# Kernel tuning notes

Measured on AMD Instinct MI355X. Metric: run time of the kernel, lower is better.

The kernel has to match this reference:

```python
import jax, jax.numpy as jnp
import numpy as np

N_EXPERTS = 8
D_HEAD = 64  # scaling dim (per-expert sub-dim)


def setup_inputs() -> dict:
    key = jax.random.key(0)
    k1, k2, k3, k4, k5, k6 = jax.random.split(key, 6)
    B, H, T, D = 2, 8, 2048, 512
    Q = jax.random.normal(k1, (B, H, T, D), dtype=jnp.float32)
    K = jax.random.normal(k2, (B, H, T, D), dtype=jnp.float32)
    V = jax.random.normal(k3, (B, H, T, D), dtype=jnp.float32)
    route_mat = jax.random.uniform(k4, (B, N_EXPERTS), dtype=jnp.float32)
    ids = jax.random.randint(k5, (B, N_EXPERTS), 0, 8, dtype=jnp.int32)
    mask = jax.random.randint(k6, (T, T), 0, 2, dtype=jnp.int32)
    return {"Q": Q, "K": K, "V": V, "route_mat": route_mat, "ids": ids, "mask": mask}


def reference(Q, K, V, route_mat, ids, mask):
    B, H, T, D = Q.shape
    E = N_EXPERTS
    ds = D // E
    # split feature dim into expert sub-slices: [B,H,T,E,ds]
    Qe = Q.reshape(B, H, T, E, ds)
    Ke = K.reshape(B, H, T, E, ds)
    Ve = V.reshape(B, H, T, E, ds)
    gate = route_mat[:, None, None, :, None]  # [B,1,1,E,1]
    # Row-parallel routed QK^T: sum over experts of gated partial products.
    dot = jnp.einsum('bhqed,bhked->bhqk', Qe * gate, Ke) / np.sqrt(D_HEAD).astype(np.float32)
    dot = jnp.where(mask[None, None, :, :].astype(bool), -jnp.inf, dot)
    attn = jax.nn.softmax(dot, axis=-1)  # dropout p=0.0 (eval)
    # Column-parallel routed score@V: per-expert output gated, concatenated along feature dim.
    Xe = jnp.einsum('bhqk,bhked->bhqed', attn, Ve) * gate
    return Xe.reshape(B, H, T, D)
```

## Files before the change

### kernel.cpp

```cpp
#include <hip/hip_runtime.h>
#include <stdint.h>

#define T_SEQ 2048
#define D_DIM 512
#define NEXP 8

typedef short bf16x8 __attribute__((ext_vector_type(8)));
typedef float floatx4 __attribute__((ext_vector_type(4)));

__device__ __forceinline__ unsigned short f2bf(float f) {
  union { float f; unsigned u; } v; v.f = f;
  return (unsigned short)((v.u + 0x7fffu + ((v.u >> 16) & 1u)) >> 16);
}

__global__ __launch_bounds__(256) void prep_k(const float* __restrict__ K,
                                              unsigned short* __restrict__ kws) {
  int idx = blockIdx.x * 256 + threadIdx.x;
  int r = idx >> 6;
  int c = idx & 63;
  const float4* src = (const float4*)(K + ((long)r << 9) + (c << 3));
  float4 a = src[0], b = src[1];
  bf16x8 v;
  v[0]=f2bf(a.x); v[1]=f2bf(a.y); v[2]=f2bf(a.z); v[3]=f2bf(a.w);
  v[4]=f2bf(b.x); v[5]=f2bf(b.y); v[6]=f2bf(b.z); v[7]=f2bf(b.w);
  int pos = (c ^ (r & 7)) << 4;
  *(bf16x8*)((char*)kws + ((long)r << 10) + pos) = v;
}

__global__ __launch_bounds__(256) void prep_vt(const float* __restrict__ V,
                                               unsigned short* __restrict__ vt) {
  __shared__ unsigned short tile[64][72];
  int bid = blockIdx.x;
  int bh = bid >> 8;
  int kt = (bid >> 3) & 31;
  int dt = bid & 7;
  int k0 = kt << 6, d0 = dt << 6;
  int tid = threadIdx.x;
  {
    int kl = tid >> 2, dc = (tid & 3) << 4;
    const float4* src = (const float4*)(V + ((long)(bh * T_SEQ + k0 + kl) << 9) + d0 + dc);
#pragma unroll
    for (int i = 0; i < 4; ++i) {
      float4 a = src[i];
      tile[kl][dc + 4*i + 0] = f2bf(a.x);
      tile[kl][dc + 4*i + 1] = f2bf(a.y);
      tile[kl][dc + 4*i + 2] = f2bf(a.z);
      tile[kl][dc + 4*i + 3] = f2bf(a.w);
    }
  }
  __syncthreads();
  {
    int dl = tid >> 2, kc = (tid & 3) << 4;
    int d = d0 + dl;
    int swz = ((d ^ (d >> 2)) & 3) << 4;
    long rowbase = (long)(bh * 512 + d) << 12;
#pragma unroll
    for (int m = 0; m < 2; ++m) {
      bf16x8 v;
#pragma unroll
      for (int j = 0; j < 8; ++j) v[j] = tile[kc + 8*m + j][dl];
      int ks = k0 + kc + 8*m;
      int pos = ((ks >> 5) << 6) + ((((ks & 31) << 1)) ^ swz);
      *(bf16x8*)((char*)vt + rowbase + pos) = v;
    }
  }
}

__global__ __launch_bounds__(512, 2) void attn_main(
    const float* __restrict__ Q, const float* __restrict__ route,
    const int* __restrict__ mask, const unsigned short* __restrict__ kws,
    const unsigned short* __restrict__ vtw, float* __restrict__ out) {
  __shared__ __align__(16) char lds[65536];
  const int tid = threadIdx.x;
  const int wq = tid >> 6;
  const int lane = tid & 63;
  const int lq = lane & 15;
  const int g = lane >> 4;
  const int bh = blockIdx.x & 15;
  const int qb = blockIdx.x >> 4;
  const int qw = qb * 128 + wq * 16;
  const int b = bh >> 3;

  float g8[NEXP];
#pragma unroll
  for (int e = 0; e < NEXP; ++e) g8[e] = route[b * NEXP + e];

  bf16x8 qa[16];
  {
    const float* qrow = Q + ((long)(bh * T_SEQ + qw + lq) << 9) + g * 8;
#pragma unroll
    for (int t = 0; t < 16; ++t) {
      const float4* p = (const float4*)(qrow + t * 32);
      float4 a = p[0], c = p[1];
      float sc = g8[t >> 1] * 0.125f;
      qa[t][0]=f2bf(a.x*sc); qa[t][1]=f2bf(a.y*sc); qa[t][2]=f2bf(a.z*sc); qa[t][3]=f2bf(a.w*sc);
      qa[t][4]=f2bf(c.x*sc); qa[t][5]=f2bf(c.y*sc); qa[t][6]=f2bf(c.z*sc); qa[t][7]=f2bf(c.w*sc);
    }
  }

  floatx4 acc[32];
#pragma unroll
  for (int n = 0; n < 32; ++n) acc[n] = 0.f;
  float mrun[4] = {-3e38f, -3e38f, -3e38f, -3e38f};
  float lrun[4] = {0.f, 0.f, 0.f, 0.f};

  const char* kbase = (const char*)kws + ((long)bh << 21);
  const char* vbase = (const char*)vtw + ((long)bh << 21);
  const int swzK = (lq & 7) << 4;
  const int swzA = ((lq ^ (lq >> 2)) & 3) << 4;

  for (int kt = 0; kt < T_SEQ / 32; ++kt) {
    const int k0 = kt * 32;
    __syncthreads();
#pragma unroll
    for (int r = 0; r < 4; ++r) {
      int row = 4 * wq + r;
      bf16x8 v = *(const bf16x8*)(kbase + ((long)(k0 + row) << 10) + lane * 16);
      *(bf16x8*)(lds + row * 1024 + lane * 16) = v;
    }
#pragma unroll
    for (int r = 0; r < 4; ++r) {
      int drow = 64 * wq + 16 * r + (lane >> 2);
      bf16x8 v = *(const bf16x8*)(vbase + ((long)drow << 12) + k0 * 2 + (lane & 3) * 16);
      *(bf16x8*)(lds + 32768 + drow * 64 + (lane & 3) * 16) = v;
    }
    __syncthreads();
    int mv0[4], mv1[4];
#pragma unroll
    for (int j = 0; j < 4; ++j) {
      long mr = (long)(qw + 4 * g + j) * T_SEQ + k0;
      mv0[j] = mask[mr + lq];
      mv1[j] = mask[mr + 16 + lq];
    }
    floatx4 s0 = 0.f, s1 = 0.f;
#pragma unroll
    for (int t = 0; t < 16; ++t) {
      int off = (t * 64 + g * 16) ^ swzK;
      bf16x8 kf0 = *(const bf16x8*)(lds + lq * 1024 + off);
      bf16x8 kf1 = *(const bf16x8*)(lds + (16 + lq) * 1024 + off);
      s0 = __builtin_amdgcn_mfma_f32_16x16x32_bf16(qa[t], kf0, s0, 0, 0, 0);
      s1 = __builtin_amdgcn_mfma_f32_16x16x32_bf16(qa[t], kf1, s1, 0, 0, 0);
    }
    __syncthreads();
    float al[4];
    int grow = 0;
#pragma unroll
    for (int j = 0; j < 4; ++j) {
      if (mv0[j]) s0[j] = -3e38f;
      if (mv1[j]) s1[j] = -3e38f;
      float tm = fmaxf(s0[j], s1[j]);
      tm = fmaxf(tm, __shfl_xor(tm, 1));
      tm = fmaxf(tm, __shfl_xor(tm, 2));
      tm = fmaxf(tm, __shfl_xor(tm, 4));
      tm = fmaxf(tm, __shfl_xor(tm, 8));
      float mn = fmaxf(mrun[j], tm);
      al[j] = __expf(mrun[j] - mn);
      grow |= (mn > mrun[j]) ? 1 : 0;
      mrun[j] = mn;
      float p0 = __expf(s0[j] - mn);
      float p1 = __expf(s1[j] - mn);
      s0[j] = p0; s1[j] = p1;
      float rs = p0 + p1;
      rs += __shfl_xor(rs, 1);
      rs += __shfl_xor(rs, 2);
      rs += __shfl_xor(rs, 4);
      rs += __shfl_xor(rs, 8);
      lrun[j] = lrun[j] * al[j] + rs;
    }
    if (__any(grow)) {
#pragma unroll
      for (int n = 0; n < 32; ++n) {
#pragma unroll
        for (int j = 0; j < 4; ++j) acc[n][j] *= al[j];
      }
    }
    char* pbase = lds + wq * 1024;
#pragma unroll
    for (int j = 0; j < 4; ++j) {
      int q = 4 * g + j;
      int swzP = ((q ^ (q >> 2)) & 3) << 4;
      *(unsigned short*)(pbase + q * 64 + ((2 * lq) ^ swzP))      = f2bf(s0[j]);
      *(unsigned short*)(pbase + q * 64 + ((32 + 2 * lq) ^ swzP)) = f2bf(s1[j]);
    }
    bf16x8 pa = *(const bf16x8*)(pbase + lq * 64 + ((16 * g) ^ swzA));
#pragma unroll
    for (int n = 0; n < 32; ++n) {
      int d = 16 * n + lq;
      int swzV = ((d ^ (d >> 2)) & 3) << 4;
      bf16x8 vb = *(const bf16x8*)(lds + 32768 + d * 64 + ((16 * g) ^ swzV));
      acc[n] = __builtin_amdgcn_mfma_f32_16x16x32_bf16(pa, vb, acc[n], 0, 0, 0);
    }
  }
  float rl[4];
#pragma unroll
  for (int j = 0; j < 4; ++j) rl[j] = 1.0f / lrun[j];
#pragma unroll
  for (int n = 0; n < 32; ++n) {
    int d = 16 * n + lq;
    float gg = g8[n >> 2];
    float* op = out + ((long)(bh * T_SEQ + qw + 4 * g) << 9) + d;
#pragma unroll
    for (int j = 0; j < 4; ++j) op[(long)j << 9] = acc[n][j] * rl[j] * gg;
  }
}

extern "C" void kernel_launch(void* const* d_in, const int* in_sizes, int n_in,
                              void* d_out, int out_size, void* d_ws, size_t ws_size,
                              hipStream_t stream) {
  (void)in_sizes; (void)n_in; (void)out_size; (void)ws_size;
  const float* Q     = (const float*)d_in[0];
  const float* K     = (const float*)d_in[1];
  const float* V     = (const float*)d_in[2];
  const float* route = (const float*)d_in[3];
  const int*   mask  = (const int*)d_in[5];
  float* out = (float*)d_out;
  unsigned short* kws = (unsigned short*)d_ws;
  unsigned short* vtw = (unsigned short*)((char*)d_ws + 33554432);
  prep_k  <<<8192, 256, 0, stream>>>(K, kws);
  prep_vt <<<4096, 256, 0, stream>>>(V, vtw);
  attn_main<<<256, 512, 0, stream>>>(Q, route, mask, kws, vtw, out);
}
```

Before: 697.9 us.

## Double-buffer K/V tiles with async global-to-LDS loads and lazy softmax rescale

Replaces the register-staged K/V tile copy with `global_load_lds` direct-to-LDS loads into two ping-pong buffers. The next tile is prefetched while the current one is computed, which cuts the per-iteration barriers from three to one and is meant to hide global memory latency. The online softmax now rescales the accumulator only when the running max grows by more than 8, avoiding most rescale passes at the cost of slightly larger unnormalized exponentials. The P scratch stride is also padded to 80 bytes, and LDS use grows to about 138KB per block.

```diff
diff --git a/kernel.cpp b/kernel.cpp
--- a/kernel.cpp
+++ b/kernel.cpp
@@ -11,6 +11,12 @@
 __device__ __forceinline__ unsigned short f2bf(float f) {
   union { float f; unsigned u; } v; v.f = f;
   return (unsigned short)((v.u + 0x7fffu + ((v.u >> 16) & 1u)) >> 16);
+}
+
+__device__ __forceinline__ void gll16(const void* gsrc, void* ldst) {
+  __builtin_amdgcn_global_load_lds(
+      (const __attribute__((address_space(1))) unsigned int*)gsrc,
+      (__attribute__((address_space(3))) unsigned int*)ldst, 16, 0, 0);
 }
 
 __global__ __launch_bounds__(256) void prep_k(const float* __restrict__ K,
@@ -70,7 +76,7 @@
     const float* __restrict__ Q, const float* __restrict__ route,
     const int* __restrict__ mask, const unsigned short* __restrict__ kws,
     const unsigned short* __restrict__ vtw, float* __restrict__ out) {
-  __shared__ __align__(16) char lds[65536];
+  __shared__ __align__(16) char lds[141312];
   const int tid = threadIdx.x;
   const int wq = tid >> 6;
   const int lane = tid & 63;
@@ -108,23 +114,39 @@
   const char* vbase = (const char*)vtw + ((long)bh << 21);
   const int swzK = (lq & 7) << 4;
   const int swzA = ((lq ^ (lq >> 2)) & 3) << 4;
+  char* pbase = lds + 131072 + wq * 1280;
+
+#define STAGE(buf, K0)                                                          \
+  {                                                                             \
+    char* kb_ = lds + (buf) * 65536;                                            \
+    char* vb_ = kb_ + 32768;                                                    \
+    _Pragma("unroll")                                                           \
+    for (int r = 0; r < 4; ++r) {                                               \
+      int row = 4 * wq + r;                                                     \
+      gll16(kbase + ((long)((K0) + row) << 10) + lane * 16, kb_ + row * 1024);  \
+    }                                                                           \
+    _Pragma("unroll")                                                           \
+    for (int r = 0; r < 4; ++r) {                                               \
+      int dr0 = 64 * wq + 16 * r;                                               \
+      gll16(vbase + ((long)(dr0 + (lane >> 2)) << 12) + (K0) * 2 + (lane & 3) * 16, \
+            vb_ + dr0 * 64);                                                    \
+    }                                                                           \
+  }
+
+  STAGE(0, 0)
+  asm volatile("s_waitcnt vmcnt(0)" ::: "memory");
+  __syncthreads();
 
   for (int kt = 0; kt < T_SEQ / 32; ++kt) {
+    const int cur = kt & 1;
     const int k0 = kt * 32;
-    __syncthreads();
-#pragma unroll
-    for (int r = 0; r < 4; ++r) {
-      int row = 4 * wq + r;
-      bf16x8 v = *(const bf16x8*)(kbase + ((long)(k0 + row) << 10) + lane * 16);
-      *(bf16x8*)(lds + row * 1024 + lane * 16) = v;
-    }
-#pragma unroll
-    for (int r = 0; r < 4; ++r) {
-      int drow = 64 * wq + 16 * r + (lane >> 2);
-      bf16x8 v = *(const bf16x8*)(vbase + ((long)drow << 12) + k0 * 2 + (lane & 3) * 16);
-      *(bf16x8*)(lds + 32768 + drow * 64 + (lane & 3) * 16) = v;
-    }
-    __syncthreads();
+    char* kb = lds + cur * 65536;
+    char* vb = kb + 32768;
+
+    if (kt + 1 < T_SEQ / 32) {
+      STAGE(cur ^ 1, k0 + 32)
+    }
+
     int mv0[4], mv1[4];
 #pragma unroll
     for (int j = 0; j < 4; ++j) {
@@ -132,17 +154,18 @@
       mv0[j] = mask[mr + lq];
       mv1[j] = mask[mr + 16 + lq];
     }
+
     floatx4 s0 = 0.f, s1 = 0.f;
 #pragma unroll
     for (int t = 0; t < 16; ++t) {
       int off = (t * 64 + g * 16) ^ swzK;
-      bf16x8 kf0 = *(const bf16x8*)(lds + lq * 1024 + off);
-      bf16x8 kf1 = *(const bf16x8*)(lds + (16 + lq) * 1024 + off);
+      bf16x8 kf0 = *(const bf16x8*)(kb + lq * 1024 + off);
+      bf16x8 kf1 = *(const bf16x8*)(kb + (16 + lq) * 1024 + off);
       s0 = __builtin_amdgcn_mfma_f32_16x16x32_bf16(qa[t], kf0, s0, 0, 0, 0);
       s1 = __builtin_amdgcn_mfma_f32_16x16x32_bf16(qa[t], kf1, s1, 0, 0, 0);
     }
-    __syncthreads();
-    float al[4];
+
+    float tmv[4];
     int grow = 0;
 #pragma unroll
     for (int j = 0; j < 4; ++j) {
@@ -153,44 +176,57 @@
       tm = fmaxf(tm, __shfl_xor(tm, 2));
       tm = fmaxf(tm, __shfl_xor(tm, 4));
       tm = fmaxf(tm, __shfl_xor(tm, 8));
-      float mn = fmaxf(mrun[j], tm);
-      al[j] = __expf(mrun[j] - mn);
-      grow |= (mn > mrun[j]) ? 1 : 0;
-      mrun[j] = mn;
-      float p0 = __expf(s0[j] - mn);
-      float p1 = __expf(s1[j] - mn);
+      tmv[j] = tm;
+      grow |= (tm > mrun[j] + 8.0f) ? 1 : 0;
+    }
+    if (__any(grow)) {
+      float al[4];
+#pragma unroll
+      for (int j = 0; j < 4; ++j) {
+        float mn = fmaxf(mrun[j], tmv[j]);
+        al[j] = __expf(mrun[j] - mn);
+        mrun[j] = mn;
+        lrun[j] *= al[j];
+      }
+#pragma unroll
+      for (int n = 0; n < 32; ++n) {
+#pragma unroll
+        for (int j = 0; j < 4; ++j) acc[n][j] *= al[j];
+      }
+    }
+#pragma unroll
+    for (int j = 0; j < 4; ++j) {
+      float p0 = __expf(s0[j] - mrun[j]);
+      float p1 = __expf(s1[j] - mrun[j]);
       s0[j] = p0; s1[j] = p1;
       float rs = p0 + p1;
       rs += __shfl_xor(rs, 1);
       rs += __shfl_xor(rs, 2);
       rs += __shfl_xor(rs, 4);
       rs += __shfl_xor(rs, 8);
-      lrun[j] = lrun[j] * al[j] + rs;
-    }
-    if (__any(grow)) {
-#pragma unroll
-      for (int n = 0; n < 32; ++n) {
-#pragma unroll
-        for (int j = 0; j < 4; ++j) acc[n][j] *= al[j];
-      }
-    }
-    char* pbase = lds + wq * 1024;
+      lrun[j] += rs;
+    }
+
 #pragma unroll
     for (int j = 0; j < 4; ++j) {
       int q = 4 * g + j;
       int swzP = ((q ^ (q >> 2)) & 3) << 4;
-      *(unsigned short*)(pbase + q * 64 + ((2 * lq) ^ swzP))      = f2bf(s0[j]);
-      *(unsigned short*)(pbase + q * 64 + ((32 + 2 * lq) ^ swzP)) = f2bf(s1[j]);
-    }
-    bf16x8 pa = *(const bf16x8*)(pbase + lq * 64 + ((16 * g) ^ swzA));
+      *(unsigned short*)(pbase + q * 80 + ((2 * lq) ^ swzP))      = f2bf(s0[j]);
+      *(unsigned short*)(pbase + q * 80 + ((32 + 2 * lq) ^ swzP)) = f2bf(s1[j]);
+    }
+    bf16x8 pa = *(const bf16x8*)(pbase + lq * 80 + ((16 * g) ^ swzA));
 #pragma unroll
     for (int n = 0; n < 32; ++n) {
       int d = 16 * n + lq;
       int swzV = ((d ^ (d >> 2)) & 3) << 4;
-      bf16x8 vb = *(const bf16x8*)(lds + 32768 + d * 64 + ((16 * g) ^ swzV));
-      acc[n] = __builtin_amdgcn_mfma_f32_16x16x32_bf16(pa, vb, acc[n], 0, 0, 0);
-    }
-  }
+      bf16x8 vb8 = *(const bf16x8*)(vb + d * 64 + ((16 * g) ^ swzV));
+      acc[n] = __builtin_amdgcn_mfma_f32_16x16x32_bf16(pa, vb8, acc[n], 0, 0, 0);
+    }
+
+    asm volatile("s_waitcnt vmcnt(0)" ::: "memory");
+    __syncthreads();
+  }
+
   float rl[4];
 #pragma unroll
   for (int j = 0; j < 4; ++j) rl[j] = 1.0f / lrun[j];
```

Measured after the change: 633.3 us. -9.3%, faster.
